# Kernel optimization log

Measured on AMD Instinct MI355X. Metric: run time of the kernel, lower is better.

Reference implementation:

```python
import jax, jax.numpy as jnp
import numpy as np


def _maxpool2x2(x):
    # x: [B, H, W, C] -> [B, H//2, W//2, C], VALID 2x2/2 max pool
    B, H, W, C = x.shape
    return x.reshape(B, H // 2, 2, W // 2, 2, C).max(axis=(2, 4))


def setup_inputs() -> dict:
    key = jax.random.key(0)
    ks = jax.random.split(key, 6)
    B, H, W, C = 16, 64, 64, 512
    x = jax.random.normal(ks[0], (B, H, W, C), dtype=jnp.float32)
    w_theta = jax.random.normal(ks[1], (C, C // 8), dtype=jnp.float32) * 0.02
    w_phi = jax.random.normal(ks[2], (C, C // 8), dtype=jnp.float32) * 0.02
    w_g = jax.random.normal(ks[3], (C, C // 2), dtype=jnp.float32) * 0.02
    w_o = jax.random.normal(ks[4], (C // 2, C), dtype=jnp.float32) * 0.02
    return {
        "x": x,
        "w_theta": w_theta, "b_theta": jnp.zeros((C // 8,), jnp.float32),
        "w_phi": w_phi, "b_phi": jnp.zeros((C // 8,), jnp.float32),
        "w_g": w_g, "b_g": jnp.zeros((C // 2,), jnp.float32),
        "w_o": w_o, "b_o": jnp.zeros((C,), jnp.float32),
        "sigma": jnp.ones((1,), jnp.float32) * 0.1,
    }


def reference(x, w_theta, b_theta, w_phi, b_phi, w_g, b_g, w_o, b_o, sigma):
    B, H, W, C = x.shape
    n_feat = H * W
    # 1x1 convs are channel-mixing GEMMs over pixels
    theta = (jnp.einsum('bhwc,cd->bhwd', x, w_theta) + b_theta).reshape(B, n_feat, C // 8)
    phi = _maxpool2x2(jnp.einsum('bhwc,cd->bhwd', x, w_phi) + b_phi).reshape(B, n_feat // 4, C // 8)
    g = _maxpool2x2(jnp.einsum('bhwc,cd->bhwd', x, w_g) + b_g).reshape(B, n_feat // 4, C // 2)
    # [B, HW, HW/4] attention (no scaling, matching SAGAN/tf source)
    attn = jax.nn.softmax(jnp.einsum('bqd,bkd->bqk', theta, phi), axis=-1)
    attn_g = jnp.einsum('bqk,bkd->bqd', attn, g).reshape(B, H, W, C // 2)
    attn_g = jnp.einsum('bhwd,dc->bhwc', attn_g, w_o) + b_o
    return x + sigma * attn_g
```

## Files before the change

kernel.cpp:

```cpp
#include <hip/hip_runtime.h>
#include <math.h>

#define NB    16
#define NPIX  4096
#define NPOOL 1024
#define CIN   512
#define CD    64
#define CG    256

typedef unsigned short u16;
typedef unsigned int   u32;
typedef __attribute__((ext_vector_type(8)))  u16    u16x8;
typedef __attribute__((ext_vector_type(8)))  __bf16 bf16x8;
typedef __attribute__((ext_vector_type(16))) float  f32x16;

__device__ __forceinline__ u16 f2bf(float x) {
    u32 u = __builtin_bit_cast(u32, x);
    u += 0x7fffu + ((u >> 16) & 1u);
    return (u16)(u >> 16);
}
__device__ __forceinline__ float bf2f(u16 h) {
    u32 u = ((u32)h) << 16;
    return __builtin_bit_cast(float, u);
}
__device__ __forceinline__ f32x16 mfma32(u16x8 a, u16x8 b, f32x16 c) {
    return __builtin_amdgcn_mfma_f32_32x32x16_bf16(
        __builtin_bit_cast(bf16x8, a), __builtin_bit_cast(bf16x8, b), c, 0, 0, 0);
}

__global__ __launch_bounds__(256) void prep_kernel(
    const float* __restrict__ wt, const float* __restrict__ wp,
    const float* __restrict__ wg, const float* __restrict__ wo,
    const float* __restrict__ bt, const float* __restrict__ bp,
    const float* __restrict__ bg,
    u16* __restrict__ WT, u16* __restrict__ WOT, float* __restrict__ biasP)
{
    const int bx = blockIdx.x;
    const int t  = threadIdx.x;

    if (bx == 320) {
        for (int i = t; i < 384; i += 256)
            biasP[i] = (i < 64) ? bt[i] : (i < 128) ? bp[i - 64] : bg[i - 128];
        return;
    }

    const float* src; u16* dst; int N, K, kt, nt;
    if (bx < 32)       { src = wt; dst = WT;             N = 64;  K = 512; kt = bx >> 1;        nt = bx & 1; }
    else if (bx < 64)  { src = wp; dst = WT + 64 * 512;  N = 64;  K = 512; kt = (bx - 32) >> 1; nt = (bx - 32) & 1; }
    else if (bx < 192) { src = wg; dst = WT + 128 * 512; N = 256; K = 512; kt = (bx - 64) >> 3; nt = (bx - 64) & 7; }
    else               { src = wo; dst = WOT;            N = 512; K = 256; kt = (bx - 192) >> 4; nt = (bx - 192) & 15; }

    __shared__ float tile[32][33];
    {
        int r  = t >> 3;
        int c4 = (t & 7) * 4;
        float4 v = *(const float4*)(src + (size_t)(kt * 32 + r) * N + nt * 32 + c4);
        tile[r][c4]     = v.x;
        tile[r][c4 + 1] = v.y;
        tile[r][c4 + 2] = v.z;
        tile[r][c4 + 3] = v.w;
    }
    __syncthreads();
    {
        int n  = t >> 3;
        int k4 = (t & 7) * 4;
        ushort4 wv;
        wv.x = f2bf(tile[k4][n]);
        wv.y = f2bf(tile[k4 + 1][n]);
        wv.z = f2bf(tile[k4 + 2][n]);
        wv.w = f2bf(tile[k4 + 3][n]);
        *(ushort4*)(dst + (size_t)(nt * 32 + n) * K + kt * 32 + k4) = wv;
    }
}

#define AST 40
__global__ __launch_bounds__(256) void proj_gemm_kernel(
    const float* __restrict__ x, const u16* __restrict__ WT,
    const float* __restrict__ biasP,
    u16* __restrict__ theta, u16* __restrict__ phiF, u16* __restrict__ gF)
{
    __shared__ u16 As[128 * AST];
    __shared__ u16 Bs[128 * AST];

    const int t  = threadIdx.x;
    const int w  = t >> 6, l = t & 63, lr = l & 31, lh = l >> 5;
    const int mt = blockIdx.x / 3, nt = blockIdx.x % 3;
    const int m0 = mt * 128, n0 = nt * 128;
    const int mw = (w & 1) * 64, nw = (w >> 1) * 64;

    const int srow = t >> 1;
    const int sks  = (t & 1) * 16;

    f32x16 acc[2][2] = {};

    for (int k0 = 0; k0 < 512; k0 += 32) {
        {
            const float4* ap = (const float4*)(x + (size_t)(m0 + srow) * 512 + k0 + sks);
            float4 v0 = ap[0], v1 = ap[1], v2 = ap[2], v3 = ap[3];
            u16x8 a0, a1;
            a0[0] = f2bf(v0.x); a0[1] = f2bf(v0.y); a0[2] = f2bf(v0.z); a0[3] = f2bf(v0.w);
            a0[4] = f2bf(v1.x); a0[5] = f2bf(v1.y); a0[6] = f2bf(v1.z); a0[7] = f2bf(v1.w);
            a1[0] = f2bf(v2.x); a1[1] = f2bf(v2.y); a1[2] = f2bf(v2.z); a1[3] = f2bf(v2.w);
            a1[4] = f2bf(v3.x); a1[5] = f2bf(v3.y); a1[6] = f2bf(v3.z); a1[7] = f2bf(v3.w);
            *(u16x8*)&As[srow * AST + sks]     = a0;
            *(u16x8*)&As[srow * AST + sks + 8] = a1;
        }
        {
            const u16x8* bp = (const u16x8*)(WT + (size_t)(n0 + srow) * 512 + k0 + sks);
            *(u16x8*)&Bs[srow * AST + sks]     = bp[0];
            *(u16x8*)&Bs[srow * AST + sks + 8] = bp[1];
        }
        __syncthreads();
#pragma unroll
        for (int ki = 0; ki < 2; ++ki) {
            u16x8 af0 = *(const u16x8*)&As[(mw + lr)      * AST + ki * 16 + lh * 8];
            u16x8 af1 = *(const u16x8*)&As[(mw + 32 + lr) * AST + ki * 16 + lh * 8];
            u16x8 bf0 = *(const u16x8*)&Bs[(nw + lr)      * AST + ki * 16 + lh * 8];
            u16x8 bf1 = *(const u16x8*)&Bs[(nw + 32 + lr) * AST + ki * 16 + lh * 8];
            acc[0][0] = mfma32(af0, bf0, acc[0][0]);
            acc[0][1] = mfma32(af0, bf1, acc[0][1]);
            acc[1][0] = mfma32(af1, bf0, acc[1][0]);
            acc[1][1] = mfma32(af1, bf1, acc[1][1]);
        }
        __syncthreads();
    }

#pragma unroll
    for (int mi = 0; mi < 2; ++mi) {
#pragma unroll
        for (int ni = 0; ni < 2; ++ni) {
            const int nb = n0 + nw + ni * 32;
            const int n  = nb + lr;
            const float bv = biasP[n];
            u16* dst; int ld, col;
            if (nb < 64)        { dst = theta; ld = 64;  col = n; }
            else if (nb < 128)  { dst = phiF;  ld = 64;  col = n - 64; }
            else                { dst = gF;    ld = 256; col = n - 128; }
#pragma unroll
            for (int r = 0; r < 16; ++r) {
                int row = m0 + mw + mi * 32 + (r & 3) + 8 * (r >> 2) + 4 * lh;
                dst[(size_t)row * ld + col] = f2bf(acc[mi][ni][r] + bv);
            }
        }
    }
}

__global__ __launch_bounds__(256) void pool_kernel(
    const u16* __restrict__ phiF, const u16* __restrict__ gF,
    u16* __restrict__ phi, u16* __restrict__ gt)
{
    const int t  = threadIdx.x;
    const int b  = blockIdx.x >> 5;
    const int ph = blockIdx.x & 31;

    {
        const int pw = t >> 3, dq = (t & 7) * 8;
        const u16* base = phiF + ((size_t)(b * NPIX + 2 * ph * 64 + 2 * pw)) * 64 + dq;
        u16x8 v00 = *(const u16x8*)(base);
        u16x8 v01 = *(const u16x8*)(base + 64);
        u16x8 v10 = *(const u16x8*)(base + 64 * 64);
        u16x8 v11 = *(const u16x8*)(base + 64 * 64 + 64);
        u16x8 m;
#pragma unroll
        for (int j = 0; j < 8; ++j) {
            float mf = fmaxf(fmaxf(bf2f(v00[j]), bf2f(v01[j])),
                             fmaxf(bf2f(v10[j]), bf2f(v11[j])));
            m[j] = f2bf(mf);
        }
        *(u16x8*)(phi + ((size_t)(b * NPOOL + ph * 32 + pw)) * 64 + dq) = m;
    }
    {
        const u16* gb = gF + ((size_t)(b * NPIX + 2 * ph * 64)) * 256 + t;
        u16 buf[32];
#pragma unroll
        for (int kp = 0; kp < 32; ++kp) {
            float m = fmaxf(
                fmaxf(bf2f(gb[(size_t)(2 * kp) * 256]),      bf2f(gb[(size_t)(2 * kp + 1) * 256])),
                fmaxf(bf2f(gb[(size_t)(64 + 2 * kp) * 256]), bf2f(gb[(size_t)(64 + 2 * kp + 1) * 256])));
            buf[kp] = f2bf(m);
        }
        u16* go = gt + ((size_t)(b * CG + t)) * NPOOL + ph * 32;
#pragma unroll
        for (int j = 0; j < 4; ++j)
            *(u16x8*)(go + j * 8) = *(const u16x8*)&buf[j * 8];
    }
}

#define SLD 1032
__global__ __launch_bounds__(256) void attn_mfma_kernel(
    const u16* __restrict__ theta, const u16* __restrict__ phi,
    const u16* __restrict__ gt, u16* __restrict__ attn_g)
{
    __shared__ u16   S[32 * SLD];
    __shared__ float rinv[32];

    const int t  = threadIdx.x;
    const int w  = t >> 6;
    const int l  = t & 63;
    const int lr = l & 31;
    const int lh = l >> 5;
    const int b  = blockIdx.x >> 7;
    const int q0 = (blockIdx.x & 127) * 32;

    const u16* thb = theta + ((size_t)(b * NPIX + q0 + lr)) * CD + lh * 8;
    u16x8 afr[4];
#pragma unroll
    for (int ki = 0; ki < 4; ++ki)
        afr[ki] = *(const u16x8*)(thb + ki * 16);

    const u16* phb = phi + (size_t)b * NPOOL * CD;
#pragma unroll 2
    for (int nt = 0; nt < 8; ++nt) {
        int k0 = w * 256 + nt * 32;
        const u16* pb = phb + (size_t)(k0 + lr) * CD + lh * 8;
        f32x16 acc = {};
#pragma unroll
        for (int ki = 0; ki < 4; ++ki)
            acc = mfma32(afr[ki], *(const u16x8*)(pb + ki * 16), acc);
#pragma unroll
        for (int r = 0; r < 16; ++r) {
            int row = (r & 3) + 8 * (r >> 2) + 4 * lh;
            S[row * SLD + k0 + lr] = f2bf(acc[r]);
        }
    }
    __syncthreads();

    {
        const int row = t >> 3, cg = t & 7;
        u16* srow = S + row * SLD;
        float mx = -1e30f;
#pragma unroll
        for (int i = 0; i < 16; ++i) {
            u16x8 v = *(const u16x8*)(srow + cg * 8 + 64 * i);
#pragma unroll
            for (int j = 0; j < 8; ++j) mx = fmaxf(mx, bf2f(v[j]));
        }
        mx = fmaxf(mx, __shfl_xor(mx, 1));
        mx = fmaxf(mx, __shfl_xor(mx, 2));
        mx = fmaxf(mx, __shfl_xor(mx, 4));
        float sum = 0.f;
#pragma unroll
        for (int i = 0; i < 16; ++i) {
            u16* p = srow + cg * 8 + 64 * i;
            u16x8 v = *(const u16x8*)p;
            u16x8 e;
#pragma unroll
            for (int j = 0; j < 8; ++j) {
                float ev = __expf(bf2f(v[j]) - mx);
                sum += ev;
                e[j] = f2bf(ev);
            }
            *(u16x8*)p = e;
        }
        sum += __shfl_xor(sum, 1);
        sum += __shfl_xor(sum, 2);
        sum += __shfl_xor(sum, 4);
        if (cg == 0) rinv[row] = 1.0f / sum;
    }
    __syncthreads();

    const u16* gtb = gt + (size_t)b * CG * NPOOL;
    const u16* gp0 = gtb + (size_t)(w * 64 + lr) * NPOOL + lh * 8;
    const u16* gp1 = gp0 + (size_t)32 * NPOOL;
    const u16* arow = S + lr * SLD + lh * 8;
    f32x16 o0 = {}, o1 = {};
#pragma unroll 4
    for (int k0 = 0; k0 < NPOOL; k0 += 16) {
        u16x8 a  = *(const u16x8*)(arow + k0);
        u16x8 b0 = *(const u16x8*)(gp0 + k0);
        u16x8 b1 = *(const u16x8*)(gp1 + k0);
        o0 = mfma32(a, b0, o0);
        o1 = mfma32(a, b1, o1);
    }

    u16* ob = attn_g + ((size_t)(b * NPIX + q0)) * CG;
#pragma unroll
    for (int r = 0; r < 16; ++r) {
        int qrow = (r & 3) + 8 * (r >> 2) + 4 * lh;
        float inv = rinv[qrow];
        ob[(size_t)qrow * CG + w * 64 + lr]      = f2bf(o0[r] * inv);
        ob[(size_t)qrow * CG + w * 64 + 32 + lr] = f2bf(o1[r] * inv);
    }
}

__global__ __launch_bounds__(256) void out_gemm_kernel(
    const u16* __restrict__ attn_gB, const u16* __restrict__ WOT,
    const float* __restrict__ x, const float* __restrict__ bo,
    const float* __restrict__ sigma, float* __restrict__ out)
{
    __shared__ u16 As[128 * AST];
    __shared__ u16 Bs[128 * AST];

    const int t  = threadIdx.x;
    const int w  = t >> 6, l = t & 63, lr = l & 31, lh = l >> 5;
    const int mt = blockIdx.x >> 2, nt = blockIdx.x & 3;
    const int m0 = mt * 128, n0 = nt * 128;
    const int mw = (w & 1) * 64, nw = (w >> 1) * 64;

    const int srow = t >> 1;
    const int sks  = (t & 1) * 16;

    f32x16 acc[2][2] = {};

    for (int k0 = 0; k0 < 256; k0 += 32) {
        {
            const u16x8* ap = (const u16x8*)(attn_gB + (size_t)(m0 + srow) * 256 + k0 + sks);
            *(u16x8*)&As[srow * AST + sks]     = ap[0];
            *(u16x8*)&As[srow * AST + sks + 8] = ap[1];
        }
        {
            const u16x8* bp = (const u16x8*)(WOT + (size_t)(n0 + srow) * 256 + k0 + sks);
            *(u16x8*)&Bs[srow * AST + sks]     = bp[0];
            *(u16x8*)&Bs[srow * AST + sks + 8] = bp[1];
        }
        __syncthreads();
#pragma unroll
        for (int ki = 0; ki < 2; ++ki) {
            u16x8 af0 = *(const u16x8*)&As[(mw + lr)      * AST + ki * 16 + lh * 8];
            u16x8 af1 = *(const u16x8*)&As[(mw + 32 + lr) * AST + ki * 16 + lh * 8];
            u16x8 bf0 = *(const u16x8*)&Bs[(nw + lr)      * AST + ki * 16 + lh * 8];
            u16x8 bf1 = *(const u16x8*)&Bs[(nw + 32 + lr) * AST + ki * 16 + lh * 8];
            acc[0][0] = mfma32(af0, bf0, acc[0][0]);
            acc[0][1] = mfma32(af0, bf1, acc[0][1]);
            acc[1][0] = mfma32(af1, bf0, acc[1][0]);
            acc[1][1] = mfma32(af1, bf1, acc[1][1]);
        }
        __syncthreads();
    }

    const float s = sigma[0];
#pragma unroll
    for (int mi = 0; mi < 2; ++mi) {
#pragma unroll
        for (int ni = 0; ni < 2; ++ni) {
            const int n  = n0 + nw + ni * 32 + lr;
            const float bv = bo[n];
#pragma unroll
            for (int r = 0; r < 16; ++r) {
                int row = m0 + mw + mi * 32 + (r & 3) + 8 * (r >> 2) + 4 * lh;
                size_t idx = (size_t)row * 512 + n;
                out[idx] = x[idx] + s * (acc[mi][ni][r] + bv);
            }
        }
    }
}

extern "C" void kernel_launch(void* const* d_in, const int* in_sizes, int n_in,
                              void* d_out, int out_size, void* d_ws, size_t ws_size,
                              hipStream_t stream)
{
    const float* x     = (const float*)d_in[0];
    const float* wt    = (const float*)d_in[1];
    const float* bt    = (const float*)d_in[2];
    const float* wp    = (const float*)d_in[3];
    const float* bp    = (const float*)d_in[4];
    const float* wg    = (const float*)d_in[5];
    const float* bg    = (const float*)d_in[6];
    const float* wo    = (const float*)d_in[7];
    const float* bo    = (const float*)d_in[8];
    const float* sigma = (const float*)d_in[9];
    float* out = (float*)d_out;

    char* ws = (char*)d_ws;
    u16*   theta   = (u16*)(ws);
    u16*   phi     = (u16*)(ws + ((size_t)8  << 20));
    u16*   phiF    = (u16*)(ws + ((size_t)10 << 20));
    u16*   gF      = (u16*)(ws + ((size_t)18 << 20));
    u16*   attn_gB = (u16*)(ws + ((size_t)10 << 20));
    u16*   gt      = (u16*)(ws + ((size_t)50 << 20));
    u16*   WT      = (u16*)(ws + ((size_t)58 << 20));
    u16*   WOT     = (u16*)(ws + ((size_t)58 << 20) + (384 << 10));
    float* biasP   = (float*)(ws + ((size_t)58 << 20) + (640 << 10));

    prep_kernel<<<321, 256, 0, stream>>>(wt, wp, wg, wo, bt, bp, bg, WT, WOT, biasP);
    proj_gemm_kernel<<<512 * 3, 256, 0, stream>>>(x, WT, biasP, theta, phiF, gF);
    pool_kernel<<<NB * 32, 256, 0, stream>>>(phiF, gF, phi, gt);
    attn_mfma_kernel<<<NB * NPIX / 32, 256, 0, stream>>>(theta, phi, gt, attn_gB);
    out_gemm_kernel<<<512 * 4, 256, 0, stream>>>(attn_gB, WOT, x, bo, sigma, out);
}
```

Before: 502.3 us.

## Swizzle block order for XCD locality and widen attention blocks to 512 threads

Remaps blockIdx in the projection, attention and output GEMM kernels so that consecutive logical tiles land on the same XCD (blockIdx & 7 selects a contiguous chunk), aiming to improve L2 reuse of shared operands such as phi, gt and weights. The attention kernel now runs 8 waves per block: each wave computes a quarter as many score tiles, the softmax uses 16 threads per row, and each wave produces 32 output channels using two independent MFMA accumulators over alternating K halves. This doubles per-block parallelism and MFMA ILP at the cost of more threads contending for the same LDS scores and higher register pressure under the 512-thread launch bound.

```diff
diff --git a/kernel.cpp b/kernel.cpp
--- a/kernel.cpp
+++ b/kernel.cpp
@@ -84,7 +84,8 @@
 
     const int t  = threadIdx.x;
     const int w  = t >> 6, l = t & 63, lr = l & 31, lh = l >> 5;
-    const int mt = blockIdx.x / 3, nt = blockIdx.x % 3;
+    const int sb = (blockIdx.x & 7) * 192 + (blockIdx.x >> 3);
+    const int mt = sb / 3, nt = sb % 3;
     const int m0 = mt * 128, n0 = nt * 128;
     const int mw = (w & 1) * 64, nw = (w >> 1) * 64;
 
@@ -187,7 +188,7 @@
 }
 
 #define SLD 1032
-__global__ __launch_bounds__(256) void attn_mfma_kernel(
+__global__ __launch_bounds__(512) void attn_mfma_kernel(
     const u16* __restrict__ theta, const u16* __restrict__ phi,
     const u16* __restrict__ gt, u16* __restrict__ attn_g)
 {
@@ -199,8 +200,9 @@
     const int l  = t & 63;
     const int lr = l & 31;
     const int lh = l >> 5;
-    const int b  = blockIdx.x >> 7;
-    const int q0 = (blockIdx.x & 127) * 32;
+    const int sb = (blockIdx.x & 7) * 256 + (blockIdx.x >> 3);
+    const int b  = sb >> 7;
+    const int q0 = (sb & 127) * 32;
 
     const u16* thb = theta + ((size_t)(b * NPIX + q0 + lr)) * CD + lh * 8;
     u16x8 afr[4];
@@ -210,8 +212,8 @@
 
     const u16* phb = phi + (size_t)b * NPOOL * CD;
 #pragma unroll 2
-    for (int nt = 0; nt < 8; ++nt) {
-        int k0 = w * 256 + nt * 32;
+    for (int nt = 0; nt < 4; ++nt) {
+        int k0 = w * 128 + nt * 32;
         const u16* pb = phb + (size_t)(k0 + lr) * CD + lh * 8;
         f32x16 acc = {};
 #pragma unroll
@@ -226,22 +228,23 @@
     __syncthreads();
 
     {
-        const int row = t >> 3, cg = t & 7;
+        const int row = t >> 4, cg = t & 15;
         u16* srow = S + row * SLD;
         float mx = -1e30f;
 #pragma unroll
-        for (int i = 0; i < 16; ++i) {
-            u16x8 v = *(const u16x8*)(srow + cg * 8 + 64 * i);
+        for (int i = 0; i < 8; ++i) {
+            u16x8 v = *(const u16x8*)(srow + cg * 8 + 128 * i);
 #pragma unroll
             for (int j = 0; j < 8; ++j) mx = fmaxf(mx, bf2f(v[j]));
         }
         mx = fmaxf(mx, __shfl_xor(mx, 1));
         mx = fmaxf(mx, __shfl_xor(mx, 2));
         mx = fmaxf(mx, __shfl_xor(mx, 4));
+        mx = fmaxf(mx, __shfl_xor(mx, 8));
         float sum = 0.f;
 #pragma unroll
-        for (int i = 0; i < 16; ++i) {
-            u16* p = srow + cg * 8 + 64 * i;
+        for (int i = 0; i < 8; ++i) {
+            u16* p = srow + cg * 8 + 128 * i;
             u16x8 v = *(const u16x8*)p;
             u16x8 e;
 #pragma unroll
@@ -255,31 +258,31 @@
         sum += __shfl_xor(sum, 1);
         sum += __shfl_xor(sum, 2);
         sum += __shfl_xor(sum, 4);
+        sum += __shfl_xor(sum, 8);
         if (cg == 0) rinv[row] = 1.0f / sum;
     }
     __syncthreads();
 
-    const u16* gtb = gt + (size_t)b * CG * NPOOL;
-    const u16* gp0 = gtb + (size_t)(w * 64 + lr) * NPOOL + lh * 8;
-    const u16* gp1 = gp0 + (size_t)32 * NPOOL;
+    const u16* gtb  = gt + (size_t)b * CG * NPOOL;
+    const u16* gp   = gtb + (size_t)(w * 32 + lr) * NPOOL + lh * 8;
     const u16* arow = S + lr * SLD + lh * 8;
-    f32x16 o0 = {}, o1 = {};
+    f32x16 oa = {}, ob2 = {};
 #pragma unroll 4
-    for (int k0 = 0; k0 < NPOOL; k0 += 16) {
-        u16x8 a  = *(const u16x8*)(arow + k0);
-        u16x8 b0 = *(const u16x8*)(gp0 + k0);
-        u16x8 b1 = *(const u16x8*)(gp1 + k0);
-        o0 = mfma32(a, b0, o0);
-        o1 = mfma32(a, b1, o1);
-    }
-
-    u16* ob = attn_g + ((size_t)(b * NPIX + q0)) * CG;
+    for (int k0 = 0; k0 < NPOOL; k0 += 32) {
+        u16x8 a0 = *(const u16x8*)(arow + k0);
+        u16x8 a1 = *(const u16x8*)(arow + k0 + 16);
+        u16x8 b0 = *(const u16x8*)(gp + k0);
+        u16x8 b1 = *(const u16x8*)(gp + k0 + 16);
+        oa  = mfma32(a0, b0, oa);
+        ob2 = mfma32(a1, b1, ob2);
+    }
+
+    u16* obp = attn_g + ((size_t)(b * NPIX + q0)) * CG;
 #pragma unroll
     for (int r = 0; r < 16; ++r) {
         int qrow = (r & 3) + 8 * (r >> 2) + 4 * lh;
         float inv = rinv[qrow];
-        ob[(size_t)qrow * CG + w * 64 + lr]      = f2bf(o0[r] * inv);
-        ob[(size_t)qrow * CG + w * 64 + 32 + lr] = f2bf(o1[r] * inv);
+        obp[(size_t)qrow * CG + w * 32 + lr] = f2bf((oa[r] + ob2[r]) * inv);
     }
 }
 
@@ -293,7 +296,8 @@
 
     const int t  = threadIdx.x;
     const int w  = t >> 6, l = t & 63, lr = l & 31, lh = l >> 5;
-    const int mt = blockIdx.x >> 2, nt = blockIdx.x & 3;
+    const int sb = (blockIdx.x & 7) * 256 + (blockIdx.x >> 3);
+    const int mt = sb >> 2, nt = sb & 3;
     const int m0 = mt * 128, n0 = nt * 128;
     const int mw = (w & 1) * 64, nw = (w >> 1) * 64;
 
@@ -375,6 +379,6 @@
     prep_kernel<<<321, 256, 0, stream>>>(wt, wp, wg, wo, bt, bp, bg, WT, WOT, biasP);
     proj_gemm_kernel<<<512 * 3, 256, 0, stream>>>(x, WT, biasP, theta, phiF, gF);
     pool_kernel<<<NB * 32, 256, 0, stream>>>(phiF, gF, phi, gt);
-    attn_mfma_kernel<<<NB * NPIX / 32, 256, 0, stream>>>(theta, phi, gt, attn_gB);
+    attn_mfma_kernel<<<NB * NPIX / 32, 512, 0, stream>>>(theta, phi, gt, attn_gB);
     out_gemm_kernel<<<512 * 4, 256, 0, stream>>>(attn_gB, WOT, x, bo, sigma, out);
 }
```

Measured after the change: 494.6 us. Within noise of the previous version (-1.5%).
